# Performance work log

Hardware: AMD Instinct MI355X
Metric: run time of the kernel (lower is better)

## Reference

```python
import jax, jax.numpy as jnp
import numpy as np

NUM_GRAPHS = 512

def setup_inputs() -> dict:
    key = jax.random.key(0)
    ks = jax.random.split(key, 16)
    N, E, F_IN, D = 50000, 800000, 128, 64
    x = jax.random.normal(ks[0], (N, F_IN), dtype=jnp.float32)
    edge_index = jax.random.randint(ks[1], (2, E), 0, N, dtype=jnp.int32)
    batch_index = jnp.sort(jax.random.randint(ks[2], (N,), 0, NUM_GRAPHS, dtype=jnp.int32))
    def lin(k, fin, fout):
        s = 1.0 / np.sqrt(fin)
        return jax.random.uniform(k, (fin, fout), jnp.float32, -s, s)
    return {
        "x": x, "edge_index": edge_index, "batch_index": batch_index,
        "W0": lin(ks[3], F_IN, D), "b0": jnp.zeros((D,), jnp.float32),
        "W1": lin(ks[4], D, D), "b1": jnp.zeros((D,), jnp.float32),
        "W2": lin(ks[5], D, D), "b2": jnp.zeros((D,), jnp.float32),
        "W3": lin(ks[6], D, D), "b3": jnp.zeros((D,), jnp.float32),
        "Wout": lin(ks[7], 2 * D, 1), "bout": jnp.zeros((1,), jnp.float32),
    }

def _gcn_edges(edge_index, N):
    # add self-loops and compute symmetric normalization D^-1/2 (A+I) D^-1/2
    loops = jnp.arange(N, dtype=edge_index.dtype)
    row = jnp.concatenate([edge_index[0], loops])  # source
    col = jnp.concatenate([edge_index[1], loops])  # target
    deg = jax.ops.segment_sum(jnp.ones_like(col, dtype=jnp.float32), col, num_segments=N)
    dinv = jnp.where(deg > 0, jax.lax.rsqrt(deg), 0.0)
    norm = dinv[row] * dinv[col]  # [E+N]
    return row, col, norm

def _gcn_conv(h, row, col, norm, W, b, N):
    h = h @ W                                   # [N, D] linear transform first
    msg = h[row] * norm[:, None]                # gather + scale
    out = jax.ops.segment_sum(msg, col, num_segments=N)  # scatter-add
    return out + b

def reference(x, edge_index, batch_index, W0, b0, W1, b1, W2, b2, W3, b3, Wout, bout):
    N = x.shape[0]
    row, col, norm = _gcn_edges(edge_index, N)
    h = jnp.tanh(_gcn_conv(x, row, col, norm, W0, b0, N))
    h = jnp.tanh(_gcn_conv(h, row, col, norm, W1, b1, N))
    h = jnp.tanh(_gcn_conv(h, row, col, norm, W2, b2, N))
    h = jnp.tanh(_gcn_conv(h, row, col, norm, W3, b3, N))
    gmax = jax.ops.segment_max(h, batch_index, num_segments=NUM_GRAPHS)
    gmax = jnp.where(jnp.isfinite(gmax), gmax, 0.0)  # empty segments -> 0
    gsum = jax.ops.segment_sum(h, batch_index, num_segments=NUM_GRAPHS)
    cnt = jax.ops.segment_sum(jnp.ones((N,), jnp.float32), batch_index, num_segments=NUM_GRAPHS)
    gmean = gsum / jnp.maximum(cnt, 1.0)[:, None]
    hidden = jnp.concatenate([gmax, gmean], axis=1)   # [G, 2D]
    out = hidden @ Wout + bout                        # [G, 1]
    return out, hidden
```

## Files before the change

### kernel.cpp

```cpp
#include <hip/hip_runtime.h>
#include <math.h>

#define CAP 64
typedef unsigned short ushort_t;
typedef unsigned int uint_t;

__global__ __launch_bounds__(256) void k_scatter2(const int* __restrict__ row,
                                                  const int* __restrict__ col, int E, int N,
                                                  int* __restrict__ deg, ushort_t* __restrict__ csr) {
    const int part = blockIdx.x & 7;
    const int slot = blockIdx.x >> 3;
    const int nslots = gridDim.x >> 3;
    const int lo = (int)((long long)N * part / 8);
    const int hi = (int)((long long)N * (part + 1) / 8);
    const int nq = E >> 2;
    for (int t = slot * blockDim.x + threadIdx.x; t < nq; t += nslots * blockDim.x) {
        int4 c = ((const int4*)col)[t];
        int4 r = ((const int4*)row)[t];
        if (c.x >= lo && c.x < hi) { int d = atomicAdd(&deg[c.x], 1); if (d < CAP) csr[((size_t)c.x << 6) + d] = (ushort_t)r.x; }
        if (c.y >= lo && c.y < hi) { int d = atomicAdd(&deg[c.y], 1); if (d < CAP) csr[((size_t)c.y << 6) + d] = (ushort_t)r.y; }
        if (c.z >= lo && c.z < hi) { int d = atomicAdd(&deg[c.z], 1); if (d < CAP) csr[((size_t)c.z << 6) + d] = (ushort_t)r.z; }
        if (c.w >= lo && c.w < hi) { int d = atomicAdd(&deg[c.w], 1); if (d < CAP) csr[((size_t)c.w << 6) + d] = (ushort_t)r.w; }
    }
    if (blockIdx.x == 0) {
        for (int e = (nq << 2) + threadIdx.x; e < E; e += blockDim.x) {
            int c = col[e];
            int d = atomicAdd(&deg[c], 1);
            if (d < CAP) csr[((size_t)c << 6) + d] = (ushort_t)row[e];
        }
    }
}

template <int K>
__global__ __launch_bounds__(256) void k_gemm(const float* __restrict__ X,
                                              const float* __restrict__ W,
                                              const int* __restrict__ deg,
                                              float* __restrict__ Gb, int N) {
    __shared__ __align__(16) float Wl[32 * 64];
    __shared__ __align__(16) float Xl[64 * 36];

    const int tid = threadIdx.x;
    const int wave = tid >> 6, lane = tid & 63;
    const int d8 = lane & 7, ns = lane >> 3;
    const int n0 = wave * 16 + ns, n1 = n0 + 8;

    const int base = blockIdx.x * 64;
    if (base >= N) return;
    const int tile_n = min(64, N - base);

    float4 a0l = {0,0,0,0}, a0h = {0,0,0,0}, a1l = {0,0,0,0}, a1h = {0,0,0,0};

    for (int kh = 0; kh < K / 32; kh++) {
        __syncthreads();
        for (int i = tid; i < 512; i += 256)
            ((float4*)Wl)[i] = ((const float4*)(W + kh * 2048))[i];
        for (int idx = tid; idx < 512; idx += 256) {
            int n = idx >> 3, q = idx & 7;
            float4 v = {0,0,0,0};
            if (n < tile_n) v = ((const float4*)(X + (size_t)(base + n) * K + kh * 32))[q];
            ((float4*)(Xl + n * 36))[q] = v;
        }
        __syncthreads();

        const float4* xq0 = (const float4*)(Xl + n0 * 36);
        const float4* xq1 = (const float4*)(Xl + n1 * 36);
        const float* wcol = Wl + d8 * 8;
#pragma unroll
        for (int kq = 0; kq < 8; kq++) {
            const float4 x4a = xq0[kq];
            const float4 x4b = xq1[kq];
            const float xs0[4] = {x4a.x, x4a.y, x4a.z, x4a.w};
            const float xs1[4] = {x4b.x, x4b.y, x4b.z, x4b.w};
#pragma unroll
            for (int j = 0; j < 4; j++) {
                const int k = kq * 4 + j;
                const float4 wa = *(const float4*)(wcol + k * 64);
                const float4 wb = *(const float4*)(wcol + k * 64 + 4);
                const float xa = xs0[j];
                const float xb = xs1[j];
                a0l.x = fmaf(xa, wa.x, a0l.x); a0l.y = fmaf(xa, wa.y, a0l.y);
                a0l.z = fmaf(xa, wa.z, a0l.z); a0l.w = fmaf(xa, wa.w, a0l.w);
                a0h.x = fmaf(xa, wb.x, a0h.x); a0h.y = fmaf(xa, wb.y, a0h.y);
                a0h.z = fmaf(xa, wb.z, a0h.z); a0h.w = fmaf(xa, wb.w, a0h.w);
                a1l.x = fmaf(xb, wa.x, a1l.x); a1l.y = fmaf(xb, wa.y, a1l.y);
                a1l.z = fmaf(xb, wa.z, a1l.z); a1l.w = fmaf(xb, wa.w, a1l.w);
                a1h.x = fmaf(xb, wb.x, a1h.x); a1h.y = fmaf(xb, wb.y, a1h.y);
                a1h.z = fmaf(xb, wb.z, a1h.z); a1h.w = fmaf(xb, wb.w, a1h.w);
            }
        }
    }

    int gn0 = base + n0, gn1 = base + n1;
    if (gn0 < N) {
        float s = rsqrtf((float)(deg[gn0] + 1));
        float4* ptr = (float4*)(Gb + (size_t)gn0 * 64);
        ptr[d8 * 2]     = make_float4(a0l.x * s, a0l.y * s, a0l.z * s, a0l.w * s);
        ptr[d8 * 2 + 1] = make_float4(a0h.x * s, a0h.y * s, a0h.z * s, a0h.w * s);
    }
    if (gn1 < N) {
        float s = rsqrtf((float)(deg[gn1] + 1));
        float4* ptr = (float4*)(Gb + (size_t)gn1 * 64);
        ptr[d8 * 2]     = make_float4(a1l.x * s, a1l.y * s, a1l.z * s, a1l.w * s);
        ptr[d8 * 2 + 1] = make_float4(a1h.x * s, a1h.y * s, a1h.z * s, a1h.w * s);
    }
}

__global__ __launch_bounds__(256) void k_agg(const float* __restrict__ Gb,
                                             const int* __restrict__ deg,
                                             const ushort_t* __restrict__ csr,
                                             const float* __restrict__ bias,
                                             float* __restrict__ H, int N) {
    const int tid = threadIdx.x;
    const int wave = tid >> 6, lane = tid & 63;
    const int s = lane >> 4;
    const int q = lane & 15;
    const int n = blockIdx.x * 16 + wave * 4 + s;
    const bool alive = (n < N);

    int cnt = 0;
    if (alive) { cnt = deg[n]; if (cnt > CAP) cnt = CAP; }
    const ushort_t* rowp = csr + ((size_t)(alive ? n : 0) << 6);

    float4 acc = {0.f, 0.f, 0.f, 0.f};
    if (alive) acc = ((const float4*)(Gb + (size_t)n * 64))[q];

    int i = 0;
    for (; i + 8 <= cnt; i += 8) {
        uint2 qa = *(const uint2*)(rowp + i);
        uint2 qb = *(const uint2*)(rowp + i + 4);
        int j0 = qa.x & 0xffff, j1 = qa.x >> 16, j2 = qa.y & 0xffff, j3 = qa.y >> 16;
        int j4 = qb.x & 0xffff, j5 = qb.x >> 16, j6 = qb.y & 0xffff, j7 = qb.y >> 16;
        float4 g0 = ((const float4*)(Gb + (size_t)j0 * 64))[q];
        float4 g1 = ((const float4*)(Gb + (size_t)j1 * 64))[q];
        float4 g2 = ((const float4*)(Gb + (size_t)j2 * 64))[q];
        float4 g3 = ((const float4*)(Gb + (size_t)j3 * 64))[q];
        float4 g4 = ((const float4*)(Gb + (size_t)j4 * 64))[q];
        float4 g5 = ((const float4*)(Gb + (size_t)j5 * 64))[q];
        float4 g6 = ((const float4*)(Gb + (size_t)j6 * 64))[q];
        float4 g7 = ((const float4*)(Gb + (size_t)j7 * 64))[q];
        float4 t0 = make_float4(g0.x + g1.x, g0.y + g1.y, g0.z + g1.z, g0.w + g1.w);
        float4 t1 = make_float4(g2.x + g3.x, g2.y + g3.y, g2.z + g3.z, g2.w + g3.w);
        float4 t2 = make_float4(g4.x + g5.x, g4.y + g5.y, g4.z + g5.z, g4.w + g5.w);
        float4 t3 = make_float4(g6.x + g7.x, g6.y + g7.y, g6.z + g7.z, g6.w + g7.w);
        acc.x += (t0.x + t1.x) + (t2.x + t3.x);
        acc.y += (t0.y + t1.y) + (t2.y + t3.y);
        acc.z += (t0.z + t1.z) + (t2.z + t3.z);
        acc.w += (t0.w + t1.w) + (t2.w + t3.w);
    }
    if (i + 4 <= cnt) {
        uint2 qa = *(const uint2*)(rowp + i);
        int j0 = qa.x & 0xffff, j1 = qa.x >> 16, j2 = qa.y & 0xffff, j3 = qa.y >> 16;
        float4 g0 = ((const float4*)(Gb + (size_t)j0 * 64))[q];
        float4 g1 = ((const float4*)(Gb + (size_t)j1 * 64))[q];
        float4 g2 = ((const float4*)(Gb + (size_t)j2 * 64))[q];
        float4 g3 = ((const float4*)(Gb + (size_t)j3 * 64))[q];
        acc.x += (g0.x + g1.x) + (g2.x + g3.x);
        acc.y += (g0.y + g1.y) + (g2.y + g3.y);
        acc.z += (g0.z + g1.z) + (g2.z + g3.z);
        acc.w += (g0.w + g1.w) + (g2.w + g3.w);
        i += 4;
    }
    if (i + 2 <= cnt) {
        uint_t qq = *(const uint_t*)(rowp + i);
        int j0 = qq & 0xffff, j1 = qq >> 16;
        float4 g0 = ((const float4*)(Gb + (size_t)j0 * 64))[q];
        float4 g1 = ((const float4*)(Gb + (size_t)j1 * 64))[q];
        acc.x += g0.x + g1.x; acc.y += g0.y + g1.y;
        acc.z += g0.z + g1.z; acc.w += g0.w + g1.w;
        i += 2;
    }
    if (i < cnt) {
        int j0 = rowp[i];
        float4 g0 = ((const float4*)(Gb + (size_t)j0 * 64))[q];
        acc.x += g0.x; acc.y += g0.y; acc.z += g0.z; acc.w += g0.w;
    }

    if (alive) {
        float dinv = rsqrtf((float)(cnt + 1));
        float4 b4 = ((const float4*)bias)[q];
        float4 r;
        r.x = tanhf(fmaf(acc.x, dinv, b4.x));
        r.y = tanhf(fmaf(acc.y, dinv, b4.y));
        r.z = tanhf(fmaf(acc.z, dinv, b4.z));
        r.w = tanhf(fmaf(acc.w, dinv, b4.w));
        ((float4*)(H + (size_t)n * 64))[q] = r;
    }
}

__global__ __launch_bounds__(256) void k_pool(const float* __restrict__ H,
                                              const int* __restrict__ batch, int N, int Gn,
                                              const float* __restrict__ Wout,
                                              const float* __restrict__ bout,
                                              float* __restrict__ out,
                                              float* __restrict__ hidden) {
    int g = blockIdx.x * 4 + (threadIdx.x >> 6);
    if (g >= Gn) return;
    int lane = threadIdx.x & 63;
    int lo = 0, hi = N;
    while (lo < hi) { int m = (lo + hi) >> 1; if (batch[m] < g) lo = m + 1; else hi = m; }
    int s = lo;
    lo = s; hi = N;
    while (lo < hi) { int m = (lo + hi) >> 1; if (batch[m] < g + 1) lo = m + 1; else hi = m; }
    int c = lo - s;

    float m0 = -INFINITY, m1 = -INFINITY, m2 = -INFINITY, m3 = -INFINITY;
    float s0 = 0.f, s1 = 0.f, s2 = 0.f, s3 = 0.f;
    int n = s;
    for (; n + 3 < s + c; n += 4) {
        float v0 = H[(size_t)n * 64 + lane];
        float v1 = H[(size_t)(n + 1) * 64 + lane];
        float v2 = H[(size_t)(n + 2) * 64 + lane];
        float v3 = H[(size_t)(n + 3) * 64 + lane];
        m0 = fmaxf(m0, v0); s0 += v0;
        m1 = fmaxf(m1, v1); s1 += v1;
        m2 = fmaxf(m2, v2); s2 += v2;
        m3 = fmaxf(m3, v3); s3 += v3;
    }
    for (; n < s + c; n++) {
        float v = H[(size_t)n * 64 + lane];
        m0 = fmaxf(m0, v); s0 += v;
    }
    float vmax = fmaxf(fmaxf(m0, m1), fmaxf(m2, m3));
    float vsum = (s0 + s1) + (s2 + s3);
    float gmax = (c > 0) ? vmax : 0.f;
    float gmean = (c > 0) ? vsum / (float)c : 0.f;
    hidden[(size_t)g * 128 + lane] = gmax;
    hidden[(size_t)g * 128 + 64 + lane] = gmean;
    float p = fmaf(gmax, Wout[lane], gmean * Wout[64 + lane]);
    for (int o = 32; o > 0; o >>= 1) p += __shfl_down(p, o);
    if (lane == 0) out[g] = p + bout[0];
}

extern "C" void kernel_launch(void* const* d_in, const int* in_sizes, int n_in,
                              void* d_out, int out_size, void* d_ws, size_t ws_size,
                              hipStream_t stream) {
    const float* x    = (const float*)d_in[0];
    const int*   ei   = (const int*)d_in[1];
    const int*   batch= (const int*)d_in[2];
    const float* W0 = (const float*)d_in[3];  const float* b0 = (const float*)d_in[4];
    const float* W1 = (const float*)d_in[5];  const float* b1 = (const float*)d_in[6];
    const float* W2 = (const float*)d_in[7];  const float* b2 = (const float*)d_in[8];
    const float* W3 = (const float*)d_in[9];  const float* b3 = (const float*)d_in[10];
    const float* Wout = (const float*)d_in[11]; const float* bout = (const float*)d_in[12];

    const int N  = in_sizes[2];
    const int E  = in_sizes[1] / 2;
    const int Gn = out_size / 129;

    const int* row = ei;
    const int* col = ei + E;

    float* out_p    = (float*)d_out;
    float* hidden_p = out_p + Gn;

    char* wp = (char*)d_ws;
    auto alloc = [&](size_t bytes) { void* p = (void*)wp; wp += (bytes + 255) & ~(size_t)255; return p; };
    int*      deg = (int*)alloc((size_t)N * 4);
    ushort_t* csr = (ushort_t*)alloc((size_t)N * CAP * 2);
    float*    Gb  = (float*)alloc((size_t)N * 64 * 4);
    float*    Hb  = (float*)alloc((size_t)N * 64 * 4);

    hipMemsetAsync(deg, 0, (size_t)N * 4, stream);
    k_scatter2<<<2048, 256, 0, stream>>>(row, col, E, N, deg, csr);

    const int gblocks = (N + 63) / 64;
    const int ablocks = (N + 15) / 16;

    k_gemm<128><<<gblocks, 256, 0, stream>>>(x, W0, deg, Gb, N);
    k_agg<<<ablocks, 256, 0, stream>>>(Gb, deg, csr, b0, Hb, N);
    k_gemm<64><<<gblocks, 256, 0, stream>>>(Hb, W1, deg, Gb, N);
    k_agg<<<ablocks, 256, 0, stream>>>(Gb, deg, csr, b1, Hb, N);
    k_gemm<64><<<gblocks, 256, 0, stream>>>(Hb, W2, deg, Gb, N);
    k_agg<<<ablocks, 256, 0, stream>>>(Gb, deg, csr, b2, Hb, N);
    k_gemm<64><<<gblocks, 256, 0, stream>>>(Hb, W3, deg, Gb, N);
    k_agg<<<ablocks, 256, 0, stream>>>(Gb, deg, csr, b3, Hb, N);

    k_pool<<<(Gn + 3) / 4, 256, 0, stream>>>(Hb, batch, N, Gn, Wout, bout, out_p, hidden_p);
}
```

Before: 330.3 us.

## Sort nodes by degree for aggregation and split pooling across four waves

```diff
diff --git a/kernel.cpp b/kernel.cpp
--- a/kernel.cpp
+++ b/kernel.cpp
@@ -28,6 +28,36 @@
             int d = atomicAdd(&deg[c], 1);
             if (d < CAP) csr[((size_t)c << 6) + d] = (ushort_t)row[e];
         }
+    }
+}
+
+__global__ __launch_bounds__(256) void k_hist(const int* __restrict__ deg, int N,
+                                              int* __restrict__ bins) {
+    __shared__ int hb[CAP + 1];
+    const int tid = threadIdx.x;
+    if (tid <= CAP) hb[tid] = 0;
+    __syncthreads();
+    for (int i = blockIdx.x * blockDim.x + tid; i < N; i += gridDim.x * blockDim.x) {
+        int d = deg[i]; if (d > CAP) d = CAP;
+        atomicAdd(&hb[d], 1);
+    }
+    __syncthreads();
+    if (tid <= CAP && hb[tid]) atomicAdd(&bins[tid], hb[tid]);
+}
+
+__global__ void k_scan(const int* __restrict__ bins, int* __restrict__ offs) {
+    if (threadIdx.x == 0) {
+        int a = 0;
+        for (int i = 0; i <= CAP; i++) { offs[i] = a; a += bins[i]; }
+    }
+}
+
+__global__ __launch_bounds__(256) void k_perm(const int* __restrict__ deg, int N,
+                                              int* __restrict__ offs, int* __restrict__ perm) {
+    for (int i = blockIdx.x * blockDim.x + threadIdx.x; i < N; i += gridDim.x * blockDim.x) {
+        int d = deg[i]; if (d > CAP) d = CAP;
+        int pos = atomicAdd(&offs[d], 1);
+        perm[pos] = i | (d << 20);
     }
 }
 
@@ -106,7 +136,7 @@
 }
 
 __global__ __launch_bounds__(256) void k_agg(const float* __restrict__ Gb,
-                                             const int* __restrict__ deg,
+                                             const int* __restrict__ perm,
                                              const ushort_t* __restrict__ csr,
                                              const float* __restrict__ bias,
                                              float* __restrict__ H, int N) {
@@ -114,12 +144,13 @@
     const int wave = tid >> 6, lane = tid & 63;
     const int s = lane >> 4;
     const int q = lane & 15;
-    const int n = blockIdx.x * 16 + wave * 4 + s;
-    const bool alive = (n < N);
-
-    int cnt = 0;
-    if (alive) { cnt = deg[n]; if (cnt > CAP) cnt = CAP; }
-    const ushort_t* rowp = csr + ((size_t)(alive ? n : 0) << 6);
+    const int slot = blockIdx.x * 16 + wave * 4 + s;
+    const bool alive = (slot < N);
+
+    const int pv = alive ? perm[slot] : 0;
+    const int n = pv & 0xFFFFF;
+    const int cnt = alive ? (pv >> 20) : 0;
+    const ushort_t* rowp = csr + ((size_t)n << 6);
 
     float4 acc = {0.f, 0.f, 0.f, 0.f};
     if (alive) acc = ((const float4*)(Gb + (size_t)n * 64))[q];
@@ -193,42 +224,52 @@
                                               const float* __restrict__ bout,
                                               float* __restrict__ out,
                                               float* __restrict__ hidden) {
-    int g = blockIdx.x * 4 + (threadIdx.x >> 6);
+    __shared__ float lm[4][64];
+    __shared__ float ls[4][64];
+    const int g = blockIdx.x;
     if (g >= Gn) return;
-    int lane = threadIdx.x & 63;
+    const int tid = threadIdx.x;
+    const int w = tid >> 6, lane = tid & 63;
+
     int lo = 0, hi = N;
     while (lo < hi) { int m = (lo + hi) >> 1; if (batch[m] < g) lo = m + 1; else hi = m; }
-    int s = lo;
-    lo = s; hi = N;
+    const int s = lo;
+    hi = N;
     while (lo < hi) { int m = (lo + hi) >> 1; if (batch[m] < g + 1) lo = m + 1; else hi = m; }
-    int c = lo - s;
+    const int c = lo - s;
+    const int e = s + c;
 
     float m0 = -INFINITY, m1 = -INFINITY, m2 = -INFINITY, m3 = -INFINITY;
     float s0 = 0.f, s1 = 0.f, s2 = 0.f, s3 = 0.f;
-    int n = s;
-    for (; n + 3 < s + c; n += 4) {
+    int n = s + w;
+    for (; n + 12 < e; n += 16) {
         float v0 = H[(size_t)n * 64 + lane];
-        float v1 = H[(size_t)(n + 1) * 64 + lane];
-        float v2 = H[(size_t)(n + 2) * 64 + lane];
-        float v3 = H[(size_t)(n + 3) * 64 + lane];
+        float v1 = H[(size_t)(n + 4) * 64 + lane];
+        float v2 = H[(size_t)(n + 8) * 64 + lane];
+        float v3 = H[(size_t)(n + 12) * 64 + lane];
         m0 = fmaxf(m0, v0); s0 += v0;
         m1 = fmaxf(m1, v1); s1 += v1;
         m2 = fmaxf(m2, v2); s2 += v2;
         m3 = fmaxf(m3, v3); s3 += v3;
     }
-    for (; n < s + c; n++) {
+    for (; n < e; n += 4) {
         float v = H[(size_t)n * 64 + lane];
         m0 = fmaxf(m0, v); s0 += v;
     }
-    float vmax = fmaxf(fmaxf(m0, m1), fmaxf(m2, m3));
-    float vsum = (s0 + s1) + (s2 + s3);
-    float gmax = (c > 0) ? vmax : 0.f;
-    float gmean = (c > 0) ? vsum / (float)c : 0.f;
-    hidden[(size_t)g * 128 + lane] = gmax;
-    hidden[(size_t)g * 128 + 64 + lane] = gmean;
-    float p = fmaf(gmax, Wout[lane], gmean * Wout[64 + lane]);
-    for (int o = 32; o > 0; o >>= 1) p += __shfl_down(p, o);
-    if (lane == 0) out[g] = p + bout[0];
+    lm[w][lane] = fmaxf(fmaxf(m0, m1), fmaxf(m2, m3));
+    ls[w][lane] = (s0 + s1) + (s2 + s3);
+    __syncthreads();
+    if (w == 0) {
+        float vmax = fmaxf(fmaxf(lm[0][lane], lm[1][lane]), fmaxf(lm[2][lane], lm[3][lane]));
+        float vsum = (ls[0][lane] + ls[1][lane]) + (ls[2][lane] + ls[3][lane]);
+        float gmax = (c > 0) ? vmax : 0.f;
+        float gmean = (c > 0) ? vsum / (float)c : 0.f;
+        hidden[(size_t)g * 128 + lane] = gmax;
+        hidden[(size_t)g * 128 + 64 + lane] = gmean;
+        float p = fmaf(gmax, Wout[lane], gmean * Wout[64 + lane]);
+        for (int o = 32; o > 0; o >>= 1) p += __shfl_down(p, o);
+        if (lane == 0) out[g] = p + bout[0];
+    }
 }
 
 extern "C" void kernel_launch(void* const* d_in, const int* in_sizes, int n_in,
@@ -255,25 +296,32 @@
 
     char* wp = (char*)d_ws;
     auto alloc = [&](size_t bytes) { void* p = (void*)wp; wp += (bytes + 255) & ~(size_t)255; return p; };
-    int*      deg = (int*)alloc((size_t)N * 4);
-    ushort_t* csr = (ushort_t*)alloc((size_t)N * CAP * 2);
-    float*    Gb  = (float*)alloc((size_t)N * 64 * 4);
-    float*    Hb  = (float*)alloc((size_t)N * 64 * 4);
+    int*      deg  = (int*)alloc((size_t)N * 4);
+    ushort_t* csr  = (ushort_t*)alloc((size_t)N * CAP * 2);
+    float*    Gb   = (float*)alloc((size_t)N * 64 * 4);
+    float*    Hb   = (float*)alloc((size_t)N * 64 * 4);
+    int*      bins = (int*)alloc((CAP + 1) * 4);
+    int*      offs = (int*)alloc((CAP + 1) * 4);
+    int*      perm = (int*)alloc((size_t)N * 4);
 
     hipMemsetAsync(deg, 0, (size_t)N * 4, stream);
+    hipMemsetAsync(bins, 0, (CAP + 1) * 4, stream);
     k_scatter2<<<2048, 256, 0, stream>>>(row, col, E, N, deg, csr);
+    k_hist<<<256, 256, 0, stream>>>(deg, N, bins);
+    k_scan<<<1, 64, 0, stream>>>(bins, offs);
+    k_perm<<<256, 256, 0, stream>>>(deg, N, offs, perm);
 
     const int gblocks = (N + 63) / 64;
     const int ablocks = (N + 15) / 16;
 
     k_gemm<128><<<gblocks, 256, 0, stream>>>(x, W0, deg, Gb, N);
-    k_agg<<<ablocks, 256, 0, stream>>>(Gb, deg, csr, b0, Hb, N);
+    k_agg<<<ablocks, 256, 0, stream>>>(Gb, perm, csr, b0, Hb, N);
     k_gemm<64><<<gblocks, 256, 0, stream>>>(Hb, W1, deg, Gb, N);
-    k_agg<<<ablocks, 256, 0, stream>>>(Gb, deg, csr, b1, Hb, N);
+    k_agg<<<ablocks, 256, 0, stream>>>(Gb, perm, csr, b1, Hb, N);
     k_gemm<64><<<gblocks, 256, 0, stream>>>(Hb, W2, deg, Gb, N);
-    k_agg<<<ablocks, 256, 0, stream>>>(Gb, deg, csr, b2, Hb, N);
+    k_agg<<<ablocks, 256, 0, stream>>>(Gb, perm, csr, b2, Hb, N);
     k_gemm<64><<<gblocks, 256, 0, stream>>>(Hb, W3, deg, Gb, N);
-    k_agg<<<ablocks, 256, 0, stream>>>(Gb, deg, csr, b3, Hb, N);
-
-    k_pool<<<(Gn + 3) / 4, 256, 0, stream>>>(Hb, batch, N, Gn, Wout, bout, out_p, hidden_p);
-}
+    k_agg<<<ablocks, 256, 0, stream>>>(Gb, perm, csr, b3, Hb, N);
+
+    k_pool<<<Gn, 256, 0, stream>>>(Hb, batch, N, Gn, Wout, bout, out_p, hidden_p);
+}
```

Measured after the change: 463.8 us. 1.4x slower.
